# Performance work log

Hardware: AMD Instinct MI355X
Metric: run time of the kernel (lower is better)

## Reference

```python
import math
import jax, jax.numpy as jnp
import numpy as np

B, S, DIM = 4, 2048, 1024
N_HEADS = 16
HEAD_DIM = DIM // N_HEADS  # 64
THETA = 10000.0


def _rope_tables(seq_len):
    # theta_of_dims = 1/theta^(2i/head_dim) for i in 0..head_dim/2
    inv = 1.0 / (THETA ** (jnp.arange(0, HEAD_DIM, 2, dtype=jnp.float32) / HEAD_DIM))
    pos = jnp.arange(seq_len, dtype=jnp.float32)[:, None]
    freqs = pos * inv  # [S, HEAD_DIM/2]
    return jnp.cos(freqs), jnp.sin(freqs)


def _apply_rope(x, cos, sin):
    # x: [B, S, H, HEAD_DIM]; complex pairs are (even, odd) interleaved
    xr = x[..., 0::2]
    xi = x[..., 1::2]
    c = cos[None, :, None, :]  # [1, S, 1, HEAD_DIM/2]
    s = sin[None, :, None, :]
    out_r = xr * c - xi * s
    out_i = xr * s + xi * c
    return jnp.stack([out_r, out_i], axis=-1).reshape(x.shape)


def setup_inputs() -> dict:
    key = jax.random.key(0)
    kx, kl, kq, kk, kv, ko = jax.random.split(key, 6)
    scale = 0.02
    return {
        "x": jax.random.normal(kx, (B, S, DIM), dtype=jnp.float32),
        "seq_lens": jax.random.randint(kl, (B,), 1, S, dtype=jnp.int32),
        "wq": jax.random.normal(kq, (DIM, DIM), dtype=jnp.float32) * scale,
        "wk": jax.random.normal(kk, (DIM, DIM), dtype=jnp.float32) * scale,
        "wv": jax.random.normal(kv, (DIM, DIM), dtype=jnp.float32) * scale,
        "wo": jax.random.normal(ko, (DIM, DIM), dtype=jnp.float32) * scale,
    }


def reference(x, seq_lens, wq, wk, wv, wo):
    b, s, _ = x.shape
    # padding mask: mask[idx, :l, l:] = -inf (rows < l cannot attend to cols >= l)
    pos = jnp.arange(s)
    l = seq_lens[:, None, None]  # [B,1,1]
    mask = jnp.where((pos[None, :, None] < l) & (pos[None, None, :] >= l),
                     -jnp.inf, 0.0).astype(jnp.float32)  # [B,S,S]

    xq = (x @ wq.T).reshape(b, s, N_HEADS, HEAD_DIM)
    xk = (x @ wk.T).reshape(b, s, N_HEADS, HEAD_DIM)
    xv = (x @ wv.T).reshape(b, s, N_HEADS, HEAD_DIM)

    cos, sin = _rope_tables(s)
    xq = _apply_rope(xq, cos, sin)
    xk = _apply_rope(xk, cos, sin)

    q = xq.transpose(0, 2, 1, 3)  # [B,H,S,D]
    k = xk.transpose(0, 2, 1, 3)
    v = xv.transpose(0, 2, 1, 3)

    scores = jnp.einsum('bhqd,bhkd->bhqk', q, k) / math.sqrt(HEAD_DIM)
    scores = scores + mask[:, None, :, :]
    probs = jax.nn.softmax(scores, axis=-1)
    out = jnp.einsum('bhqk,bhkd->bhqd', probs, v)  # [B,H,S,D]
    out = out.transpose(0, 2, 1, 3).reshape(b, s, DIM)
    return out @ wo.T
```

## Files before the change

kernel.cpp:

```cpp
#include <hip/hip_runtime.h>
#include <hip/hip_bf16.h>
#include <stdint.h>


typedef __attribute__((ext_vector_type(8))) short s8v;
typedef __attribute__((ext_vector_type(2))) float f2v;
typedef __attribute__((ext_vector_type(4))) float f4v;
typedef __attribute__((ext_vector_type(16))) float f16v;

#define GLL16(gsrc, ldst) __builtin_amdgcn_global_load_lds(              \
    (const __attribute__((address_space(1))) void*)(gsrc),               \
    (__attribute__((address_space(3))) void*)(ldst), 16, 0, 0)

__device__ __forceinline__ short f2bf(float f) {
  union { float f; unsigned i; } v; v.f = f;
  unsigned r = v.i + 0x7fffu + ((v.i >> 16) & 1u);
  return (short)(r >> 16);
}
__device__ __forceinline__ unsigned cvtpk(float a, float b) {
  unsigned r;
  asm("v_cvt_pk_bf16_f32 %0, %1, %2" : "=v"(r) : "v"(a), "v"(b));
  return r;
}

__global__ void k_rope(float* __restrict__ ct, float* __restrict__ st) {
  int idx = blockIdx.x * 256 + threadIdx.x;
  int pos = idx >> 5, i = idx & 31;
  float inv = exp2f(-13.287712379549449f * ((float)i / 32.0f));
  float a = (float)pos * inv;
  float s, c;
  sincosf(a, &s, &c);
  ct[idx] = c; st[idx] = s;
}

__global__ void k_cvt(const float* __restrict__ in, short* __restrict__ out, int n4) {
  int i = blockIdx.x * 256 + threadIdx.x;
  if (i >= n4) return;
  float4 v = ((const float4*)in)[i];
  short4 o;
  o.x = f2bf(v.x); o.y = f2bf(v.y); o.z = f2bf(v.z); o.w = f2bf(v.w);
  ((short4*)out)[i] = o;
}

__global__ __launch_bounds__(256, 2) void k_gemm_qkv(
    const short* __restrict__ xb, const short* __restrict__ wb,
    const float* __restrict__ ct, const float* __restrict__ st,
    short* __restrict__ qb, short* __restrict__ kb, short* __restrict__ vt)
{
  __shared__ short As[2][128 * 64];
  __shared__ short Bs[2][128 * 64];
  const int bid = blockIdx.x;
  const int item = (bid & 7) * 192 + (bid >> 3);
  const int row_m = (item & 63) * 128;
  const int row_n = (item >> 6) * 128;
  const int tid = threadIdx.x;
  const int lane = tid & 63, w = tid >> 6;
  const int g = lane >> 4, lq = lane & 15;
  const int wm = (w >> 1) * 64, wn = (w & 1) * 64;
  const int srow = tid >> 3;
  const int schunk = (lane & 7) ^ ((lane >> 3) & 7);

  f4v acc[4][4];
#pragma unroll
  for (int i = 0; i < 4; i++)
#pragma unroll
    for (int j = 0; j < 4; j++) acc[i][j] = f4v{0.f, 0.f, 0.f, 0.f};

  auto stage = [&](int kt, int s) {
#pragma unroll
    for (int j = 0; j < 4; j++)
      GLL16(xb + (size_t)(row_m + j * 32 + srow) * 1024 + kt + schunk * 8,
            &As[s][j * 2048 + w * 512]);
#pragma unroll
    for (int j = 0; j < 4; j++)
      GLL16(wb + (size_t)(row_n + j * 32 + srow) * 1024 + kt + schunk * 8,
            &Bs[s][j * 2048 + w * 512]);
  };

  stage(0, 0);
  stage(64, 1);
  asm volatile("s_waitcnt vmcnt(8)" ::: "memory");
  __builtin_amdgcn_sched_barrier(0);
  asm volatile("s_barrier" ::: "memory");

  for (int t = 0; t < 16; t++) {
    const int s = t & 1;
    const short* Ac = &As[s][0];
    const short* Bc = &Bs[s][0];
#pragma unroll
    for (int kk = 0; kk < 2; kk++) {
      s8v a[4], b[4];
#pragma unroll
      for (int mi = 0; mi < 4; mi++) {
        const int r_ = wm + mi * 16 + lq;
        a[mi] = *(const s8v*)&Ac[r_ * 64 + (((kk * 4 + g) ^ (lq & 7)) * 8)];
      }
#pragma unroll
      for (int ni = 0; ni < 4; ni++) {
        const int r_ = wn + ni * 16 + lq;
        b[ni] = *(const s8v*)&Bc[r_ * 64 + (((kk * 4 + g) ^ (lq & 7)) * 8)];
      }
      __builtin_amdgcn_s_setprio(1);
#pragma unroll
      for (int mi = 0; mi < 4; mi++)
#pragma unroll
        for (int ni = 0; ni < 4; ni++)
          acc[mi][ni] = __builtin_amdgcn_mfma_f32_16x16x32_bf16(a[mi], b[ni], acc[mi][ni], 0, 0, 0);
      __builtin_amdgcn_s_setprio(0);
    }
    if (t < 15) {
      asm volatile("s_waitcnt lgkmcnt(0)" ::: "memory");
      asm volatile("s_barrier" ::: "memory");
      if (t < 14) {
        stage((t + 2) * 64, s);
        asm volatile("s_waitcnt vmcnt(8)" ::: "memory");
      } else {
        asm volatile("s_waitcnt vmcnt(0)" ::: "memory");
      }
      __builtin_amdgcn_sched_barrier(0);
      asm volatile("s_barrier" ::: "memory");
    }
  }

  const int sel = row_n >> 10;
  if (sel < 2) {
    short* __restrict__ dst = (sel == 0) ? qb : kb;
#pragma unroll
    for (int mi = 0; mi < 4; mi++) {
#pragma unroll
      for (int ni = 0; ni < 4; ni++) {
        const int o = row_n + wn + ni * 16 + lq;
        const int oin = o & 1023, h = oin >> 6, d = oin & 63;
#pragma unroll
        for (int r = 0; r < 4; r++) {
          const int tt = row_m + wm + mi * 16 + g * 4 + r;
          const int b_ = tt >> 11, s_ = tt & 2047;
          float v = acc[mi][ni][r];
          float p = __shfl_xor(v, 1);
          const int i2 = d >> 1;
          const float cv = ct[s_ * 32 + i2], sv = st[s_ * 32 + i2];
          float outv = (d & 1) ? fmaf(p, sv, v * cv) : fmaf(-p, sv, v * cv);
          dst[((size_t)(b_ * 16 + h) * 2048 + s_) * 64 + d] = f2bf(outv);
        }
      }
    }
  } else {
#pragma unroll
    for (int mi = 0; mi < 4; mi++) {
#pragma unroll
      for (int ni = 0; ni < 4; ni++) {
        const int o = row_n + wn + ni * 16 + lq;
        const int oin = o & 1023, h = oin >> 6, d = oin & 63;
        const int t0 = row_m + wm + mi * 16 + g * 4;
        const int b_ = t0 >> 11, s_ = t0 & 2047;
        short4 pk;
        pk.x = f2bf(acc[mi][ni][0]); pk.y = f2bf(acc[mi][ni][1]);
        pk.z = f2bf(acc[mi][ni][2]); pk.w = f2bf(acc[mi][ni][3]);
        *(short4*)&vt[((size_t)(b_ * 16 + h) * 64 + d) * 2048 + s_] = pk;
      }
    }
  }
}

__global__ __launch_bounds__(512, 4) void k_attn(
    const short* __restrict__ qb, const short* __restrict__ kb, const short* __restrict__ vt,
    const int* __restrict__ seq_lens, short* __restrict__ ao)
{
  __shared__ short Ks[2][64 * 64];
  __shared__ short Vs[2][64 * 64];
  __shared__ short Es[8][32 * 72];
  const int n = blockIdx.x;
  const int bh = (n & 7) * 8 + ((n >> 3) & 7);
  const int qblk = n >> 6;
  const int b = bh >> 4, h = bh & 15;
  const int tid = threadIdx.x, lane = tid & 63, w = tid >> 6;
  const int lq32 = lane & 31, hl = lane >> 5;
  const int L = seq_lens[b];
  const int q0 = qblk * 256 + w * 32;
  const int lr = lane >> 3, sc = (lane & 7) ^ (lr & 7);

  const short* kbase = kb + (size_t)bh * 2048 * 64;
  const short* vbase = vt + (size_t)bh * 64 * 2048;

  const short* qsrc = qb + ((size_t)bh * 2048 + q0 + lq32) * 64 + 8 * hl;
  s8v qf[4];
#pragma unroll
  for (int ki = 0; ki < 4; ki++) qf[ki] = *(const s8v*)&qsrc[16 * ki];

  f2v lacc[8];
#pragma unroll
  for (int i = 0; i < 8; i++) lacc[i] = f2v{0.f, 0.f};
  f16v O[2];
  O[0] = f16v{0.f,0.f,0.f,0.f,0.f,0.f,0.f,0.f,0.f,0.f,0.f,0.f,0.f,0.f,0.f,0.f};
  O[1] = O[0];

  const bool blk_below = (qblk * 256 + 255) < L;
  const int nt_end = blk_below ? ((L + 63) & ~63) : 2048;
  const bool wave_below = (q0 + 31) < L;
  const float CSC = 0.18033688011112042f;
  const float nmc = -32.0f * CSC;
  const int qp = q0 + lq32;
  const int rsw = (lq32 & 7);
  short* pw = &Es[w][0];

  GLL16(kbase + (size_t)(w * 8 + lr) * 64 + sc * 8, &Ks[0][w * 512]);
  GLL16(vbase + (size_t)(w * 8 + lr) * 2048 + sc * 8, &Vs[0][w * 512]);

  int cur = 0;
  for (int t0 = 0; t0 < nt_end; t0 += 64) {
    if (t0 + 64 < nt_end) {
      const int tn = t0 + 64;
      GLL16(kbase + (size_t)(tn + w * 8 + lr) * 64 + sc * 8, &Ks[cur ^ 1][w * 512]);
      GLL16(vbase + (size_t)(w * 8 + lr) * 2048 + tn + sc * 8, &Vs[cur ^ 1][w * 512]);
      asm volatile("s_waitcnt vmcnt(2)" ::: "memory");
    } else {
      asm volatile("s_waitcnt vmcnt(0)" ::: "memory");
    }
    __builtin_amdgcn_sched_barrier(0);
    asm volatile("s_barrier" ::: "memory");

    if (!(wave_below && t0 >= L)) {
      const short* Kc = &Ks[cur][0];
      const short* Vc = &Vs[cur][0];

      f16v sa[2];
      __builtin_amdgcn_s_setprio(1);
#pragma unroll
      for (int sub = 0; sub < 2; sub++) {
        f16v acc = f16v{0.f,0.f,0.f,0.f,0.f,0.f,0.f,0.f,0.f,0.f,0.f,0.f,0.f,0.f,0.f,0.f};
#pragma unroll
        for (int ki = 0; ki < 4; ki++) {
          s8v kf = *(const s8v*)&Kc[(sub * 32 + lq32) * 64 + (((2 * ki + hl) ^ rsw) * 8)];
          acc = __builtin_amdgcn_mfma_f32_32x32x16_bf16(kf, qf[ki], acc, 0, 0, 0);
        }
        sa[sub] = acc;
      }
      __builtin_amdgcn_s_setprio(0);

      const bool nomask = (t0 + 64 <= L) || (q0 >= L);
      if (!nomask) {
        const bool qfree = (qp >= L);
#pragma unroll
        for (int sub = 0; sub < 2; sub++)
#pragma unroll
          for (int r = 0; r < 16; r++) {
            const int kvp = t0 + sub * 32 + (r & 3) + 8 * (r >> 2) + 4 * hl;
            if (!(qfree || kvp < L)) sa[sub][r] = -1e30f;
          }
      }

#pragma unroll
      for (int sub = 0; sub < 2; sub++)
#pragma unroll
        for (int r = 0; r < 16; r++)
          sa[sub][r] = __builtin_amdgcn_exp2f(fmaf(sa[sub][r], CSC, nmc));
#pragma unroll
      for (int r8 = 0; r8 < 8; r8++) {
        f2v a = f2v{sa[0][2 * r8], sa[0][2 * r8 + 1]};
        f2v c = f2v{sa[1][2 * r8], sa[1][2 * r8 + 1]};
        lacc[r8] += a + c;
      }

#pragma unroll
      for (int sub = 0; sub < 2; sub++)
#pragma unroll
        for (int j = 0; j < 4; j++) {
          uint2 u;
          u.x = cvtpk(sa[sub][4 * j],     sa[sub][4 * j + 1]);
          u.y = cvtpk(sa[sub][4 * j + 2], sa[sub][4 * j + 3]);
          const int kvo = sub * 32 + 8 * j + 4 * hl;
          *(uint2*)&pw[lq32 * 72 + kvo] = u;
        }
      asm volatile("" ::: "memory");

      __builtin_amdgcn_s_setprio(1);
#pragma unroll
      for (int sub = 0; sub < 2; sub++) {
        s8v pa = *(const s8v*)&pw[lq32 * 72 + sub * 32 + hl * 8];
        s8v pb = *(const s8v*)&pw[lq32 * 72 + sub * 32 + 16 + hl * 8];
#pragma unroll
        for (int dt = 0; dt < 2; dt++) {
          s8v vf0 = *(const s8v*)&Vc[(32 * dt + lq32) * 64 + (((4 * sub + hl) ^ rsw) * 8)];
          O[dt] = __builtin_amdgcn_mfma_f32_32x32x16_bf16(vf0, pa, O[dt], 0, 0, 0);
          s8v vf1 = *(const s8v*)&Vc[(32 * dt + lq32) * 64 + (((4 * sub + 2 + hl) ^ rsw) * 8)];
          O[dt] = __builtin_amdgcn_mfma_f32_32x32x16_bf16(vf1, pb, O[dt], 0, 0, 0);
        }
      }
      __builtin_amdgcn_s_setprio(0);
    }
    asm volatile("s_barrier" ::: "memory");
    cur ^= 1;
  }

  f2v l2 = (lacc[0] + lacc[1]) + (lacc[2] + lacc[3]);
  f2v l3 = (lacc[4] + lacc[5]) + (lacc[6] + lacc[7]);
  l2 += l3;
  float l_run = l2.x + l2.y;
  l_run += __shfl_xor(l_run, 32);
  const float inv = 1.0f / l_run;
  short* es = &Es[w][0];
#pragma unroll
  for (int dt = 0; dt < 2; dt++)
#pragma unroll
    for (int rp = 0; rp < 8; rp++) {
      unsigned u = cvtpk(O[dt][2 * rp] * inv, O[dt][2 * rp + 1] * inv);
      const int dbase = 8 * (rp >> 1) + 2 * (rp & 1);
      *(unsigned*)&es[lq32 * 72 + 32 * dt + dbase + 4 * hl] = u;
    }
  asm volatile("" ::: "memory");
#pragma unroll
  for (int pph = 0; pph < 4; pph++) {
    const int qq = pph * 8 + lr;
    s8v vv = *(const s8v*)&es[qq * 72 + (lane & 7) * 8];
    *(s8v*)&ao[((size_t)b * 2048 + q0 + qq) * 1024 + h * 64 + (lane & 7) * 8] = vv;
  }
}

__global__ __launch_bounds__(256, 2) void k_gemm_out(
    const short* __restrict__ ab, const short* __restrict__ wob, float* __restrict__ out)
{
  __shared__ short As[2][128 * 64];
  __shared__ short Bs[2][128 * 64];
  const int bid = blockIdx.x;
  const int item = (bid & 7) * 64 + (bid >> 3);
  const int row_m = (item & 63) * 128;
  const int row_n = (item >> 6) * 128;
  const int tid = threadIdx.x;
  const int lane = tid & 63, w = tid >> 6;
  const int g = lane >> 4, lq = lane & 15;
  const int wm = (w >> 1) * 64, wn = (w & 1) * 64;
  const int srow = tid >> 3;
  const int schunk = (lane & 7) ^ ((lane >> 3) & 7);

  f4v acc[4][4];
#pragma unroll
  for (int i = 0; i < 4; i++)
#pragma unroll
    for (int j = 0; j < 4; j++) acc[i][j] = f4v{0.f, 0.f, 0.f, 0.f};

  auto stage = [&](int kt, int s) {
#pragma unroll
    for (int j = 0; j < 4; j++)
      GLL16(ab + (size_t)(row_m + j * 32 + srow) * 1024 + kt + schunk * 8,
            &As[s][j * 2048 + w * 512]);
#pragma unroll
    for (int j = 0; j < 4; j++)
      GLL16(wob + (size_t)(row_n + j * 32 + srow) * 1024 + kt + schunk * 8,
            &Bs[s][j * 2048 + w * 512]);
  };

  stage(0, 0);
  stage(64, 1);
  asm volatile("s_waitcnt vmcnt(8)" ::: "memory");
  __builtin_amdgcn_sched_barrier(0);
  asm volatile("s_barrier" ::: "memory");

  for (int t = 0; t < 16; t++) {
    const int s = t & 1;
    const short* Ac = &As[s][0];
    const short* Bc = &Bs[s][0];
#pragma unroll
    for (int kk = 0; kk < 2; kk++) {
      s8v a[4], b[4];
#pragma unroll
      for (int mi = 0; mi < 4; mi++) {
        const int r_ = wm + mi * 16 + lq;
        a[mi] = *(const s8v*)&Ac[r_ * 64 + (((kk * 4 + g) ^ (lq & 7)) * 8)];
      }
#pragma unroll
      for (int ni = 0; ni < 4; ni++) {
        const int r_ = wn + ni * 16 + lq;
        b[ni] = *(const s8v*)&Bc[r_ * 64 + (((kk * 4 + g) ^ (lq & 7)) * 8)];
      }
      __builtin_amdgcn_s_setprio(1);
#pragma unroll
      for (int mi = 0; mi < 4; mi++)
#pragma unroll
        for (int ni = 0; ni < 4; ni++)
          acc[mi][ni] = __builtin_amdgcn_mfma_f32_16x16x32_bf16(a[mi], b[ni], acc[mi][ni], 0, 0, 0);
      __builtin_amdgcn_s_setprio(0);
    }
    if (t < 15) {
      asm volatile("s_waitcnt lgkmcnt(0)" ::: "memory");
      asm volatile("s_barrier" ::: "memory");
      if (t < 14) {
        stage((t + 2) * 64, s);
        asm volatile("s_waitcnt vmcnt(8)" ::: "memory");
      } else {
        asm volatile("s_waitcnt vmcnt(0)" ::: "memory");
      }
      __builtin_amdgcn_sched_barrier(0);
      asm volatile("s_barrier" ::: "memory");
    }
  }

#pragma unroll
  for (int mi = 0; mi < 4; mi++)
#pragma unroll
    for (int ni = 0; ni < 4; ni++) {
      const int o = row_n + wn + ni * 16 + lq;
#pragma unroll
      for (int r = 0; r < 4; r++) {
        const int tt = row_m + wm + mi * 16 + g * 4 + r;
        out[(size_t)tt * 1024 + o] = acc[mi][ni][r];
      }
    }
}

extern "C" void kernel_launch(void* const* d_in, const int* in_sizes, int n_in,
                              void* d_out, int out_size, void* d_ws, size_t ws_size,
                              hipStream_t stream) {
  const float* x  = (const float*)d_in[0];
  const int*   sl = (const int*)d_in[1];
  const float* wq = (const float*)d_in[2];
  const float* wk = (const float*)d_in[3];
  const float* wv = (const float*)d_in[4];
  const float* wo = (const float*)d_in[5];
  float* out = (float*)d_out;

  char* ws = (char*)d_ws;
  float* ct   = (float*)(ws + 0);
  float* st   = (float*)(ws + 262144);
  short* xb   = (short*)(ws + 524288);
  short* wqkv = (short*)(ws + 17301504);
  short* wob  = (short*)(ws + 23592960);
  short* qb   = (short*)(ws + 25690112);
  short* kbf  = (short*)(ws + 42467328);
  short* vtb  = (short*)(ws + 76021760);
  short* ab   = (short*)(ws + 92798976);

  k_rope<<<256, 256, 0, stream>>>(ct, st);
  k_cvt<<<8192, 256, 0, stream>>>(x, xb, 2097152);
  k_cvt<<<1024, 256, 0, stream>>>(wq, wqkv, 262144);
  k_cvt<<<1024, 256, 0, stream>>>(wk, wqkv + 1048576, 262144);
  k_cvt<<<1024, 256, 0, stream>>>(wv, wqkv + 2097152, 262144);
  k_cvt<<<1024, 256, 0, stream>>>(wo, wob, 262144);
  k_gemm_qkv<<<1536, 256, 0, stream>>>(xb, wqkv, ct, st, qb, kbf, vtb);
  k_attn<<<512, 512, 0, stream>>>(qb, kbf, vtb, sl, ab);
  k_gemm_out<<<512, 256, 0, stream>>>(ab, wob, out);
}
```

Before: 204.6 us.

## Keep attention P in registers via permlane swap, fold scale into Q, halve blocks

```diff
diff --git a/kernel.cpp b/kernel.cpp
--- a/kernel.cpp
+++ b/kernel.cpp
@@ -21,6 +21,9 @@
   unsigned r;
   asm("v_cvt_pk_bf16_f32 %0, %1, %2" : "=v"(r) : "v"(a), "v"(b));
   return r;
+}
+__device__ __forceinline__ void plswap(unsigned& x, unsigned& y) {
+  asm volatile("v_permlane32_swap_b32 %0, %1" : "+v"(x), "+v"(y));
 }
 
 __global__ void k_rope(float* __restrict__ ct, float* __restrict__ st) {
@@ -124,6 +127,7 @@
 
   const int sel = row_n >> 10;
   if (sel < 2) {
+    const float qsc = (sel == 0) ? 0.18033688011112042f : 1.0f;
     short* __restrict__ dst = (sel == 0) ? qb : kb;
 #pragma unroll
     for (int mi = 0; mi < 4; mi++) {
@@ -140,7 +144,7 @@
           const int i2 = d >> 1;
           const float cv = ct[s_ * 32 + i2], sv = st[s_ * 32 + i2];
           float outv = (d & 1) ? fmaf(p, sv, v * cv) : fmaf(-p, sv, v * cv);
-          dst[((size_t)(b_ * 16 + h) * 2048 + s_) * 64 + d] = f2bf(outv);
+          dst[((size_t)(b_ * 16 + h) * 2048 + s_) * 64 + d] = f2bf(outv * qsc);
         }
       }
     }
@@ -162,21 +166,20 @@
   }
 }
 
-__global__ __launch_bounds__(512, 4) void k_attn(
+__global__ __launch_bounds__(256, 4) void k_attn(
     const short* __restrict__ qb, const short* __restrict__ kb, const short* __restrict__ vt,
     const int* __restrict__ seq_lens, short* __restrict__ ao)
 {
-  __shared__ short Ks[2][64 * 64];
-  __shared__ short Vs[2][64 * 64];
-  __shared__ short Es[8][32 * 72];
+  __shared__ short KV[16384];
   const int n = blockIdx.x;
-  const int bh = (n & 7) * 8 + ((n >> 3) & 7);
-  const int qblk = n >> 6;
+  const int m = n >> 3;
+  const int bh = (n & 7) * 8 + (m & 7);
+  const int qblk = m >> 3;
   const int b = bh >> 4, h = bh & 15;
   const int tid = threadIdx.x, lane = tid & 63, w = tid >> 6;
   const int lq32 = lane & 31, hl = lane >> 5;
   const int L = seq_lens[b];
-  const int q0 = qblk * 256 + w * 32;
+  const int q0 = qblk * 128 + w * 32;
   const int lr = lane >> 3, sc = (lane & 7) ^ (lr & 7);
 
   const short* kbase = kb + (size_t)bh * 2048 * 64;
@@ -194,25 +197,30 @@
   O[0] = f16v{0.f,0.f,0.f,0.f,0.f,0.f,0.f,0.f,0.f,0.f,0.f,0.f,0.f,0.f,0.f,0.f};
   O[1] = O[0];
 
-  const bool blk_below = (qblk * 256 + 255) < L;
+  const bool blk_below = (qblk * 128 + 127) < L;
   const int nt_end = blk_below ? ((L + 63) & ~63) : 2048;
   const bool wave_below = (q0 + 31) < L;
-  const float CSC = 0.18033688011112042f;
-  const float nmc = -32.0f * CSC;
   const int qp = q0 + lq32;
   const int rsw = (lq32 & 7);
-  short* pw = &Es[w][0];
-
-  GLL16(kbase + (size_t)(w * 8 + lr) * 64 + sc * 8, &Ks[0][w * 512]);
-  GLL16(vbase + (size_t)(w * 8 + lr) * 2048 + sc * 8, &Vs[0][w * 512]);
+
+#pragma unroll
+  for (int i = 0; i < 2; i++) {
+    const int c = w * 2 + i;
+    GLL16(kbase + (size_t)(c * 8 + lr) * 64 + sc * 8, &KV[c * 512]);
+    GLL16(vbase + (size_t)(c * 8 + lr) * 2048 + sc * 8, &KV[8192 + c * 512]);
+  }
 
   int cur = 0;
   for (int t0 = 0; t0 < nt_end; t0 += 64) {
     if (t0 + 64 < nt_end) {
       const int tn = t0 + 64;
-      GLL16(kbase + (size_t)(tn + w * 8 + lr) * 64 + sc * 8, &Ks[cur ^ 1][w * 512]);
-      GLL16(vbase + (size_t)(w * 8 + lr) * 2048 + tn + sc * 8, &Vs[cur ^ 1][w * 512]);
-      asm volatile("s_waitcnt vmcnt(2)" ::: "memory");
+#pragma unroll
+      for (int i = 0; i < 2; i++) {
+        const int c = w * 2 + i;
+        GLL16(kbase + (size_t)(tn + c * 8 + lr) * 64 + sc * 8, &KV[(cur ^ 1) * 4096 + c * 512]);
+        GLL16(vbase + (size_t)(c * 8 + lr) * 2048 + tn + sc * 8, &KV[8192 + (cur ^ 1) * 4096 + c * 512]);
+      }
+      asm volatile("s_waitcnt vmcnt(4)" ::: "memory");
     } else {
       asm volatile("s_waitcnt vmcnt(0)" ::: "memory");
     }
@@ -220,8 +228,8 @@
     asm volatile("s_barrier" ::: "memory");
 
     if (!(wave_below && t0 >= L)) {
-      const short* Kc = &Ks[cur][0];
-      const short* Vc = &Vs[cur][0];
+      const short* Kc = &KV[cur * 4096];
+      const short* Vc = &KV[8192 + cur * 4096];
 
       f16v sa[2];
       __builtin_amdgcn_s_setprio(1);
@@ -253,7 +261,7 @@
       for (int sub = 0; sub < 2; sub++)
 #pragma unroll
         for (int r = 0; r < 16; r++)
-          sa[sub][r] = __builtin_amdgcn_exp2f(fmaf(sa[sub][r], CSC, nmc));
+          sa[sub][r] = __builtin_amdgcn_exp2f(sa[sub][r]);
 #pragma unroll
       for (int r8 = 0; r8 < 8; r8++) {
         f2v a = f2v{sa[0][2 * r8], sa[0][2 * r8 + 1]};
@@ -261,29 +269,31 @@
         lacc[r8] += a + c;
       }
 
-#pragma unroll
-      for (int sub = 0; sub < 2; sub++)
-#pragma unroll
-        for (int j = 0; j < 4; j++) {
-          uint2 u;
-          u.x = cvtpk(sa[sub][4 * j],     sa[sub][4 * j + 1]);
-          u.y = cvtpk(sa[sub][4 * j + 2], sa[sub][4 * j + 3]);
-          const int kvo = sub * 32 + 8 * j + 4 * hl;
-          *(uint2*)&pw[lq32 * 72 + kvo] = u;
-        }
-      asm volatile("" ::: "memory");
-
       __builtin_amdgcn_s_setprio(1);
 #pragma unroll
       for (int sub = 0; sub < 2; sub++) {
-        s8v pa = *(const s8v*)&pw[lq32 * 72 + sub * 32 + hl * 8];
-        s8v pb = *(const s8v*)&pw[lq32 * 72 + sub * 32 + 16 + hl * 8];
+        unsigned c0 = cvtpk(sa[sub][0],  sa[sub][1]);
+        unsigned c1 = cvtpk(sa[sub][2],  sa[sub][3]);
+        unsigned c2 = cvtpk(sa[sub][4],  sa[sub][5]);
+        unsigned c3 = cvtpk(sa[sub][6],  sa[sub][7]);
+        plswap(c0, c2);
+        plswap(c1, c3);
+        unsigned c4 = cvtpk(sa[sub][8],  sa[sub][9]);
+        unsigned c5 = cvtpk(sa[sub][10], sa[sub][11]);
+        unsigned c6 = cvtpk(sa[sub][12], sa[sub][13]);
+        unsigned c7 = cvtpk(sa[sub][14], sa[sub][15]);
+        plswap(c4, c6);
+        plswap(c5, c7);
+        union P8 { unsigned u[4]; s8v s; };
+        P8 pa, pb;
+        pa.u[0] = c0; pa.u[1] = c1; pa.u[2] = c2; pa.u[3] = c3;
+        pb.u[0] = c4; pb.u[1] = c5; pb.u[2] = c6; pb.u[3] = c7;
 #pragma unroll
         for (int dt = 0; dt < 2; dt++) {
           s8v vf0 = *(const s8v*)&Vc[(32 * dt + lq32) * 64 + (((4 * sub + hl) ^ rsw) * 8)];
-          O[dt] = __builtin_amdgcn_mfma_f32_32x32x16_bf16(vf0, pa, O[dt], 0, 0, 0);
+          O[dt] = __builtin_amdgcn_mfma_f32_32x32x16_bf16(vf0, pa.s, O[dt], 0, 0, 0);
           s8v vf1 = *(const s8v*)&Vc[(32 * dt + lq32) * 64 + (((4 * sub + 2 + hl) ^ rsw) * 8)];
-          O[dt] = __builtin_amdgcn_mfma_f32_32x32x16_bf16(vf1, pb, O[dt], 0, 0, 0);
+          O[dt] = __builtin_amdgcn_mfma_f32_32x32x16_bf16(vf1, pb.s, O[dt], 0, 0, 0);
         }
       }
       __builtin_amdgcn_s_setprio(0);
@@ -298,21 +308,23 @@
   float l_run = l2.x + l2.y;
   l_run += __shfl_xor(l_run, 32);
   const float inv = 1.0f / l_run;
-  short* es = &Es[w][0];
+  short* es = &KV[w * 2048];
 #pragma unroll
   for (int dt = 0; dt < 2; dt++)
 #pragma unroll
     for (int rp = 0; rp < 8; rp++) {
       unsigned u = cvtpk(O[dt][2 * rp] * inv, O[dt][2 * rp + 1] * inv);
-      const int dbase = 8 * (rp >> 1) + 2 * (rp & 1);
-      *(unsigned*)&es[lq32 * 72 + 32 * dt + dbase + 4 * hl] = u;
+      const int col = 32 * dt + 8 * (rp >> 1) + 2 * (rp & 1) + 4 * hl;
+      const int chunk = col >> 3, within = col & 7;
+      *(unsigned*)&es[lq32 * 64 + ((chunk ^ (lq32 & 7)) << 3) + within] = u;
     }
   asm volatile("" ::: "memory");
 #pragma unroll
   for (int pph = 0; pph < 4; pph++) {
     const int qq = pph * 8 + lr;
-    s8v vv = *(const s8v*)&es[qq * 72 + (lane & 7) * 8];
-    *(s8v*)&ao[((size_t)b * 2048 + q0 + qq) * 1024 + h * 64 + (lane & 7) * 8] = vv;
+    const int ch = lane & 7;
+    s8v vv = *(const s8v*)&es[qq * 64 + ((ch ^ lr) << 3)];
+    *(s8v*)&ao[((size_t)b * 2048 + q0 + qq) * 1024 + h * 64 + ch * 8] = vv;
   }
 }
 
@@ -436,6 +448,6 @@
   k_cvt<<<1024, 256, 0, stream>>>(wv, wqkv + 2097152, 262144);
   k_cvt<<<1024, 256, 0, stream>>>(wo, wob, 262144);
   k_gemm_qkv<<<1536, 256, 0, stream>>>(xb, wqkv, ct, st, qb, kbf, vtb);
-  k_attn<<<512, 512, 0, stream>>>(qb, kbf, vtb, sl, ab);
+  k_attn<<<1024, 256, 0, stream>>>(qb, kbf, vtb, sl, ab);
   k_gemm_out<<<512, 256, 0, stream>>>(ab, wob, out);
 }
```

New measurement: 205.0 us. Within noise of the previous version (+0.2%).
